# Performance work log

Measured on AMD Instinct MI355X. Metric: run time of the kernel, lower is better.

The kernel has to match this reference:

```python
import jax, jax.numpy as jnp
import numpy as np

SEQ_LEN = 16
N_NODES = 64000
N_EDGES = 1024000
FEAT = 16
H1 = 64
H2 = 64
LSTM_DIM = 128
FC1 = 64
FC2 = 3


def setup_inputs() -> dict:
    key = jax.random.key(0)
    ks = jax.random.split(key, 16)
    def w(k, shape, fan_in):
        return (jax.random.normal(k, shape, jnp.float32) / np.float32(np.sqrt(fan_in)))
    return {
        "x": jax.random.normal(ks[0], (N_NODES, FEAT), jnp.float32),
        "edge_attr": jax.random.uniform(ks[1], (N_EDGES, 1), jnp.float32),
        "W1": w(ks[2], (FEAT, H1), FEAT),
        "b1": jnp.zeros((H1,), jnp.float32),
        "W2": w(ks[3], (H1, H2), H1),
        "b2": jnp.zeros((H2,), jnp.float32),
        "W_ih": w(ks[4], (4 * LSTM_DIM, H2), H2),
        "W_hh": w(ks[5], (4 * LSTM_DIM, LSTM_DIM), LSTM_DIM),
        "b_ih": jnp.zeros((4 * LSTM_DIM,), jnp.float32),
        "b_hh": jnp.zeros((4 * LSTM_DIM,), jnp.float32),
        "fw1": w(ks[6], (LSTM_DIM, FC1), LSTM_DIM),
        "fb1": jnp.zeros((FC1,), jnp.float32),
        "fw2": w(ks[7], (FC1, FC2), FC1),
        "fb2": jnp.zeros((FC2,), jnp.float32),
        "edge_index": jax.random.randint(ks[8], (2, N_EDGES), 0, N_NODES, dtype=jnp.int64),
        "batch_size": 8,
    }


def gcn_conv(x, edge_index, ew, W, b):
    # PyG GCNConv with edge_weight: add self-loops (weight 1), symmetric norm.
    n = x.shape[0]
    row, col = edge_index[0], edge_index[1]
    lin = x @ W                                        # [N, H]
    deg = jax.ops.segment_sum(ew, col, num_segments=n) + 1.0  # self-loop weight 1
    dinv = jax.lax.rsqrt(deg)
    norm = dinv[row] * ew * dinv[col]                  # [E]
    agg = jax.ops.segment_sum(norm[:, None] * lin[row], col, num_segments=n)
    agg = agg + lin * (dinv * dinv)[:, None]           # self-loop term: 1/deg
    return agg + b


def lstm_last(x, W_ih, W_hh, b_ih, b_hh):
    # x: [B, T, D]; torch LSTM gate order i, f, g, o. Returns last hidden [B, H].
    B = x.shape[0]
    H = W_hh.shape[1]
    xg = jnp.einsum('btd,gd->btg', x, W_ih) + (b_ih + b_hh)  # [B, T, 4H]
    def step(carry, g_t):
        h, c = carry
        g = g_t + h @ W_hh.T
        i, f, gg, o = jnp.split(g, 4, axis=-1)
        c = jax.nn.sigmoid(f) * c + jax.nn.sigmoid(i) * jnp.tanh(gg)
        h = jax.nn.sigmoid(o) * jnp.tanh(c)
        return (h, c), None
    h0 = jnp.zeros((B, H), x.dtype)
    (h, _), _ = jax.lax.scan(step, (h0, h0), xg.transpose(1, 0, 2))
    return h


def reference(x, edge_attr, W1, b1, W2, b2, W_ih, W_hh, b_ih, b_hh,
              fw1, fb1, fw2, fb2, edge_index, batch_size):
    ew = edge_attr[:, 0]
    out = gcn_conv(x, edge_index, ew, W1, b1)
    out = jax.nn.relu(out)                 # dropout: identity in eval
    out = gcn_conv(out, edge_index, ew, W2, b2)
    out = jax.nn.relu(out)
    out = out.reshape(-1, SEQ_LEN, out.shape[-1])      # [B*S, T, H2]
    h = lstm_last(out, W_ih, W_hh, b_ih, b_hh)          # [B*S, LSTM]
    h = h.reshape(batch_size, -1, LSTM_DIM)             # [B, S, LSTM]
    h = jax.nn.relu(h @ fw1 + fb1)
    logits = h @ fw2 + fb2
    return jax.nn.softmax(logits, axis=2)
```

## Files before the change

kernel.cpp:

```cpp
#include <hip/hip_runtime.h>
#include <hip/hip_bf16.h>
#include <hip/hip_fp16.h>
#include <math.h>

#define NN 64000
#define NE 1024000
#define NB 4000
#define NT 16
#define LROWS 16
#define NBKT 250

typedef __attribute__((ext_vector_type(8))) short short8;
typedef __attribute__((ext_vector_type(4))) float f32x4;

__device__ __forceinline__ float fsigm(float x) {
    return __builtin_amdgcn_rcpf(1.0f + __expf(-x));
}
__device__ __forceinline__ float ftanh(float x) {
    return 1.0f - 2.0f * __builtin_amdgcn_rcpf(1.0f + __expf(2.0f * x));
}
__device__ __forceinline__ unsigned short hbits(float v) {
    __half h = __float2half(v);
    return reinterpret_cast<unsigned short&>(h);
}
__device__ __forceinline__ float hval(unsigned short b) {
    __half h;
    reinterpret_cast<unsigned short&>(h) = b;
    return __half2float(h);
}

__global__ __launch_bounds__(256) void k_zero256(int* __restrict__ p) {
    p[threadIdx.x] = 0;
}

__global__ __launch_bounds__(256) void k_bhist(const int* __restrict__ ei,
                                               int* __restrict__ bcnt) {
    __shared__ int h[256];
    int tid = threadIdx.x;
    h[tid] = 0;
    __syncthreads();
    int base = blockIdx.x * 4096;
    #pragma unroll
    for (int j = 0; j < 16; ++j) {
        int c = ei[NE + base + j * 256 + tid];
        atomicAdd(&h[c >> 8], 1);
    }
    __syncthreads();
    if (tid < NBKT && h[tid]) atomicAdd(&bcnt[tid], h[tid]);
}

__global__ __launch_bounds__(256) void k_bscan(const int* __restrict__ bcnt,
                                               int* __restrict__ bbase,
                                               int* __restrict__ bcur) {
    __shared__ int sm[256];
    int tid = threadIdx.x;
    int v = (tid < NBKT) ? bcnt[tid] : 0;
    sm[tid] = v;
    __syncthreads();
    #pragma unroll
    for (int d = 1; d < 256; d <<= 1) {
        int t = (tid >= d) ? sm[tid - d] : 0;
        __syncthreads();
        sm[tid] += t;
        __syncthreads();
    }
    if (tid < NBKT) { int ex = sm[tid] - v; bbase[tid] = ex; bcur[tid] = ex; }
    if (tid == 255) bbase[NBKT] = sm[255];
}

__global__ __launch_bounds__(256) void k_bin(const int* __restrict__ ei,
                                             const float* __restrict__ ew,
                                             int* __restrict__ bcur,
                                             uint2* __restrict__ binned) {
    __shared__ uint2 stage[4096];
    __shared__ int sm[256];
    __shared__ int lofs[256], lcur[256], ladj[256];
    int tid = threadIdx.x;
    sm[tid] = 0;
    __syncthreads();
    int base = blockIdx.x * 4096;
    int cs[16];
    #pragma unroll
    for (int j = 0; j < 16; ++j) {
        cs[j] = ei[NE + base + j * 256 + tid];
        atomicAdd(&sm[cs[j] >> 8], 1);
    }
    __syncthreads();
    int v = sm[tid];
    #pragma unroll
    for (int d = 1; d < 256; d <<= 1) {
        int t = (tid >= d) ? sm[tid - d] : 0;
        __syncthreads();
        sm[tid] += t;
        __syncthreads();
    }
    int ex = sm[tid] - v;
    lofs[tid] = ex;
    lcur[tid] = ex;
    if (tid < NBKT) ladj[tid] = atomicAdd(&bcur[tid], v) - ex;
    __syncthreads();
    #pragma unroll
    for (int j = 0; j < 16; ++j) {
        int e = base + j * 256 + tid;
        int c = cs[j];
        int b = c >> 8;
        unsigned r = (unsigned)ei[e];
        float wv = ew[e];
        int slot = atomicAdd(&lcur[b], 1);
        stage[slot] = make_uint2(r | ((unsigned)(c & 255) << 16) | ((unsigned)b << 24),
                                 __float_as_uint(wv));
    }
    __syncthreads();
    #pragma unroll
    for (int j = 0; j < 16; ++j) {
        int i = j * 256 + tid;
        uint2 rec = stage[i];
        int b = rec.x >> 24;
        binned[ladj[b] + i] = rec;
    }
}

__global__ __launch_bounds__(256) void k_csr(const uint2* __restrict__ binned,
                                             const int* __restrict__ bbase,
                                             unsigned* __restrict__ edata,
                                             int* __restrict__ off,
                                             float* __restrict__ dinv) {
    __shared__ int cnt[256];
    __shared__ float sumw[256];
    __shared__ int lcur[256];
    __shared__ int sm[256];
    int tid = threadIdx.x;
    int b = blockIdx.x;
    int s = bbase[b], e1 = bbase[b + 1];
    cnt[tid] = 0;
    sumw[tid] = 0.0f;
    __syncthreads();
    for (int i = s + tid; i < e1; i += 256) {
        uint2 rec = binned[i];
        int nl = (rec.x >> 16) & 255;
        atomicAdd(&cnt[nl], 1);
        atomicAdd(&sumw[nl], __uint_as_float(rec.y));
    }
    __syncthreads();
    int v = cnt[tid];
    sm[tid] = v;
    __syncthreads();
    #pragma unroll
    for (int d = 1; d < 256; d <<= 1) {
        int t = (tid >= d) ? sm[tid - d] : 0;
        __syncthreads();
        sm[tid] += t;
        __syncthreads();
    }
    int ex = sm[tid] - v;
    off[b * 256 + tid] = s + ex;
    dinv[b * 256 + tid] = rsqrtf(1.0f + sumw[tid]);
    lcur[tid] = ex;
    if (b == 0 && tid == 0) off[NN] = NE;
    __syncthreads();
    for (int i = s + tid; i < e1; i += 256) {
        uint2 rec = binned[i];
        int nl = (rec.x >> 16) & 255;
        int p = atomicAdd(&lcur[nl], 1);
        edata[s + p] = (rec.x & 0xFFFFu) |
                       ((unsigned)hbits(__uint_as_float(rec.y)) << 16);
    }
}

__global__ __launch_bounds__(256) void k_xh(const float* __restrict__ x,
                                            const float* __restrict__ dinv,
                                            __half* __restrict__ xh) {
    int i = blockIdx.x * 256 + threadIdx.x;
    int n = i >> 4;
    xh[i] = __float2half(x[i] * dinv[n]);
}

__global__ __launch_bounds__(256) void k_gather16(const __half* __restrict__ xh,
                                                  const unsigned* __restrict__ edata,
                                                  const int* __restrict__ off,
                                                  const float* __restrict__ dinv,
                                                  __half* __restrict__ aggx) {
    int tid = threadIdx.x;
    int lane = tid & 63;
    int wv = tid >> 6;
    int n = blockIdx.x * 4 + wv;
    int g = lane >> 3;
    int fl = lane & 7;
    const __half2* xh2 = (const __half2*)xh;
    float2 acc = make_float2(0.0f, 0.0f);
    if (g == 0) acc = __half22float2(xh2[((size_t)n << 3) + fl]);
    int s = off[n], e1 = off[n + 1];
    int e = s + g;
    for (; e + 8 < e1; e += 16) {
        unsigned d0 = edata[e];
        unsigned d1 = edata[e + 8];
        float2 l0 = __half22float2(xh2[((size_t)(d0 & 0xFFFFu) << 3) + fl]);
        float2 l1 = __half22float2(xh2[((size_t)(d1 & 0xFFFFu) << 3) + fl]);
        float w0 = hval((unsigned short)(d0 >> 16));
        float w1 = hval((unsigned short)(d1 >> 16));
        acc.x = fmaf(w0, l0.x, acc.x); acc.y = fmaf(w0, l0.y, acc.y);
        acc.x = fmaf(w1, l1.x, acc.x); acc.y = fmaf(w1, l1.y, acc.y);
    }
    if (e < e1) {
        unsigned d0 = edata[e];
        float2 l0 = __half22float2(xh2[((size_t)(d0 & 0xFFFFu) << 3) + fl]);
        float w0 = hval((unsigned short)(d0 >> 16));
        acc.x = fmaf(w0, l0.x, acc.x);
        acc.y = fmaf(w0, l0.y, acc.y);
    }
    acc.x += __shfl_xor(acc.x, 8, 64);
    acc.y += __shfl_xor(acc.y, 8, 64);
    acc.x += __shfl_xor(acc.x, 16, 64);
    acc.y += __shfl_xor(acc.y, 16, 64);
    acc.x += __shfl_xor(acc.x, 32, 64);
    acc.y += __shfl_xor(acc.y, 32, 64);
    if (g == 0) {
        float dn = dinv[n];
        ((__half2*)aggx)[((size_t)n << 3) + fl] = __floats2half2_rn(dn * acc.x, dn * acc.y);
    }
}

__global__ __launch_bounds__(256) void k_wgcn(const float* __restrict__ W1,
                                              const float* __restrict__ W2,
                                              unsigned short* __restrict__ W1f,
                                              unsigned short* __restrict__ W2f) {
    int i = blockIdx.x * 256 + threadIdx.x;
    if (i < 2048) {
        int j = i & 7, l = (i >> 3) & 63, nt = i >> 9;
        int n = nt * 16 + (l & 15);
        int k = ((l >> 4) << 3) + j;
        W1f[i] = (k < 16) ? hbits(W1[k * 64 + n]) : (unsigned short)0;
    } else if (i < 6144) {
        int i2 = i - 2048;
        int j = i2 & 7, l = (i2 >> 3) & 63, ci = i2 >> 9;
        int nt = ci & 3, ks = ci >> 2;
        int n = nt * 16 + (l & 15);
        int k = ks * 32 + ((l >> 4) << 3) + j;
        W2f[i2] = hbits(W2[k * 64 + n]);
    }
}

__global__ __launch_bounds__(256) void k_lin2f(const __half* __restrict__ aggx,
                                               const unsigned short* __restrict__ W1f,
                                               const float* __restrict__ b1,
                                               const unsigned short* __restrict__ W2f,
                                               const float* __restrict__ dinv,
                                               __half* __restrict__ linp2) {
    __shared__ unsigned short Ax[4][512];
    __shared__ unsigned short Hd[4][2][512];
    __shared__ unsigned short Ot[64 * 64];
    int tid = threadIdx.x;
    int lane = tid & 63;
    int w = tid >> 6;
    int n0 = blockIdx.x * 64;

    short8 B1[4], B2[8];
    #pragma unroll
    for (int nt = 0; nt < 4; ++nt) B1[nt] = *(const short8*)&W1f[nt * 512 + lane * 8];
    #pragma unroll
    for (int ci = 0; ci < 8; ++ci) B2[ci] = *(const short8*)&W2f[ci * 512 + lane * 8];

    {
        int idx = tid;
        ((unsigned int*)Ax)[(idx >> 7) * 256 + 128 + (idx & 127)] = 0;
        idx += 256;
        ((unsigned int*)Ax)[(idx >> 7) * 256 + 128 + (idx & 127)] = 0;
    }
    {
        int row = tid >> 2, k0 = (tid & 3) * 4;
        uint2 bits = *(const uint2*)(aggx + (size_t)(n0 + row) * 16 + k0);
        unsigned short hv[4] = {(unsigned short)(bits.x & 0xFFFF), (unsigned short)(bits.x >> 16),
                                (unsigned short)(bits.y & 0xFFFF), (unsigned short)(bits.y >> 16)};
        int wq = row >> 4, m = row & 15;
        #pragma unroll
        for (int d = 0; d < 4; ++d) {
            int k = k0 + d;
            Ax[wq][(((k >> 3) << 4) + m) * 8 + (k & 7)] = hv[d];
        }
    }
    __syncthreads();

    short8 a = *(const short8*)&Ax[w][lane * 8];
    f32x4 acc[4];
    #pragma unroll
    for (int nt = 0; nt < 4; ++nt) acc[nt] = (f32x4){0.f, 0.f, 0.f, 0.f};
    #pragma unroll
    for (int nt = 0; nt < 4; ++nt)
        acc[nt] = __builtin_amdgcn_mfma_f32_16x16x32_f16(a, B1[nt], acc[nt], 0, 0, 0);

    int rb = (lane >> 4) * 4;
    #pragma unroll
    for (int nt = 0; nt < 4; ++nt) {
        int col = nt * 16 + (lane & 15);
        float bc = b1[col];
        #pragma unroll
        for (int q = 0; q < 4; ++q) {
            float hv = fmaxf(acc[nt][q] + bc, 0.0f);
            int row = rb + q;
            Hd[w][col >> 5][((((col & 31) >> 3) << 4) + row) * 8 + (col & 7)] = hbits(hv);
        }
    }
    short8 a0 = *(const short8*)&Hd[w][0][lane * 8];
    short8 a1 = *(const short8*)&Hd[w][1][lane * 8];
    f32x4 c2[4];
    #pragma unroll
    for (int nt = 0; nt < 4; ++nt) c2[nt] = (f32x4){0.f, 0.f, 0.f, 0.f};
    #pragma unroll
    for (int nt = 0; nt < 4; ++nt)
        c2[nt] = __builtin_amdgcn_mfma_f32_16x16x32_f16(a0, B2[nt], c2[nt], 0, 0, 0);
    #pragma unroll
    for (int nt = 0; nt < 4; ++nt)
        c2[nt] = __builtin_amdgcn_mfma_f32_16x16x32_f16(a1, B2[4 + nt], c2[nt], 0, 0, 0);

    float dv[4];
    #pragma unroll
    for (int q = 0; q < 4; ++q) dv[q] = dinv[n0 + w * 16 + rb + q];
    #pragma unroll
    for (int nt = 0; nt < 4; ++nt) {
        int col = nt * 16 + (lane & 15);
        #pragma unroll
        for (int q = 0; q < 4; ++q) {
            Ot[(w * 16 + rb + q) * 64 + col] = hbits(c2[nt][q] * dv[q]);
        }
    }
    __syncthreads();
    {
        int row = tid >> 2, c0 = (tid & 3) * 16;
        short8 v0 = *(const short8*)&Ot[row * 64 + c0];
        short8 v1 = *(const short8*)&Ot[row * 64 + c0 + 8];
        *(short8*)&linp2[(size_t)(n0 + row) * 64 + c0] = v0;
        *(short8*)&linp2[(size_t)(n0 + row) * 64 + c0 + 8] = v1;
    }
}

__global__ __launch_bounds__(256) void k_gather(const __half* __restrict__ linp,
                                                const unsigned* __restrict__ edata,
                                                const int* __restrict__ off,
                                                const float* __restrict__ dinv,
                                                const float* __restrict__ bvec,
                                                __half* __restrict__ agg) {
    int tid = threadIdx.x;
    int lane = tid & 63;
    int wv = tid >> 6;
    int n = blockIdx.x * 4 + wv;
    int hf = lane >> 5;
    int fl = lane & 31;
    const __half2* lp2 = (const __half2*)linp;
    float2 acc = make_float2(0.0f, 0.0f);
    if (hf == 0) {
        acc = __half22float2(lp2[((size_t)n << 5) + fl]);
    }
    int s = off[n], e1 = off[n + 1];
    int e = s + hf;
    for (; e + 6 < e1; e += 8) {
        unsigned d0 = edata[e];
        unsigned d1 = edata[e + 2];
        unsigned d2 = edata[e + 4];
        unsigned d3 = edata[e + 6];
        float2 l0 = __half22float2(lp2[((size_t)(d0 & 0xFFFFu) << 5) + fl]);
        float2 l1 = __half22float2(lp2[((size_t)(d1 & 0xFFFFu) << 5) + fl]);
        float2 l2 = __half22float2(lp2[((size_t)(d2 & 0xFFFFu) << 5) + fl]);
        float2 l3 = __half22float2(lp2[((size_t)(d3 & 0xFFFFu) << 5) + fl]);
        float w0 = hval((unsigned short)(d0 >> 16));
        float w1 = hval((unsigned short)(d1 >> 16));
        float w2 = hval((unsigned short)(d2 >> 16));
        float w3 = hval((unsigned short)(d3 >> 16));
        acc.x = fmaf(w0, l0.x, acc.x); acc.y = fmaf(w0, l0.y, acc.y);
        acc.x = fmaf(w1, l1.x, acc.x); acc.y = fmaf(w1, l1.y, acc.y);
        acc.x = fmaf(w2, l2.x, acc.x); acc.y = fmaf(w2, l2.y, acc.y);
        acc.x = fmaf(w3, l3.x, acc.x); acc.y = fmaf(w3, l3.y, acc.y);
    }
    for (; e < e1; e += 2) {
        unsigned d0 = edata[e];
        float2 l0 = __half22float2(lp2[((size_t)(d0 & 0xFFFFu) << 5) + fl]);
        float w0 = hval((unsigned short)(d0 >> 16));
        acc.x = fmaf(w0, l0.x, acc.x);
        acc.y = fmaf(w0, l0.y, acc.y);
    }
    acc.x += __shfl_xor(acc.x, 32, 64);
    acc.y += __shfl_xor(acc.y, 32, 64);
    if (hf == 0) {
        float dn = dinv[n];
        float ox = fmaxf(fmaf(dn, acc.x, bvec[fl * 2]), 0.0f);
        float oy = fmaxf(fmaf(dn, acc.y, bvec[fl * 2 + 1]), 0.0f);
        ((__half2*)agg)[((size_t)n << 5) + fl] = __floats2half2_rn(ox, oy);
    }
}

__global__ __launch_bounds__(256) void k_wfrag(const float* __restrict__ W_ih,
                                               const float* __restrict__ W_hh,
                                               const float* __restrict__ b_ih,
                                               const float* __restrict__ b_hh,
                                               unsigned short* __restrict__ Bus,
                                               float* __restrict__ biasb) {
    int i = blockIdx.x * 256 + threadIdx.x;
    if (i < 192 * 512) {
        int j = i & 7;
        int l = (i >> 3) & 63;
        int ci = i >> 9;
        int ntg = ci & 31;
        int ks = ci >> 5;
        int col = ntg * 16 + (l & 15);
        int k = ks * 32 + ((l >> 4) << 3) + j;
        float w = (k < 64) ? W_ih[col * 64 + k] : W_hh[col * 128 + (k - 64)];
        Bus[i] = hbits(w);
    }
    if (i < 512) biasb[i] = b_ih[i] + b_hh[i];
}

__global__ __launch_bounds__(512, 2) void k_lstm(const unsigned short* __restrict__ seq,
                                                 const unsigned short* __restrict__ Bus,
                                                 const float* __restrict__ biasb,
                                                 float* __restrict__ hout) {
    __shared__ unsigned short Aus[6 * 512];
    int tid = threadIdx.x;
    int lane = tid & 63;
    int w = tid >> 6;
    int b0 = blockIdx.x * LROWS;

    int u = w * 16 + (lane & 15);
    int rbase = (lane >> 4) * 4;
    float bI = biasb[u], bF = biasb[128 + u], bG = biasb[256 + u], bO = biasb[384 + u];
    float cst[4] = {0.0f, 0.0f, 0.0f, 0.0f};

    short8 Bf[24];
    #pragma unroll
    for (int ks = 0; ks < 6; ++ks) {
        #pragma unroll
        for (int g = 0; g < 4; ++g) {
            int ci = ks * 32 + 8 * g + w;
            Bf[ks * 4 + g] = *(const short8*)&Bus[(size_t)ci * 512 + lane * 8];
        }
    }

    for (int i = tid; i < 1024; i += 512) ((unsigned int*)Aus)[512 + i] = 0;
    {
        int i0 = tid * 2;
        int row = i0 >> 6, k0 = i0 & 63;
        unsigned v = *(const unsigned*)&seq[((size_t)(b0 + row) * NT + 0) * 64 + k0];
        int ks = k0 >> 5, kr = k0 & 31;
        Aus[ks * 512 + (((kr >> 3) << 4) + row) * 8 + (kr & 7)] = (unsigned short)v;
        kr = (k0 + 1) & 31; ks = (k0 + 1) >> 5;
        Aus[ks * 512 + (((kr >> 3) << 4) + row) * 8 + (kr & 7)] = (unsigned short)(v >> 16);
    }
    __syncthreads();

    for (int t = 0; t < NT; ++t) {
        f32x4 acc[4];
        #pragma unroll
        for (int g = 0; g < 4; ++g) acc[g] = (f32x4){0.f, 0.f, 0.f, 0.f};
        #pragma unroll
        for (int ks = 0; ks < 6; ++ks) {
            short8 ah = *(const short8*)&Aus[ks * 512 + lane * 8];
            #pragma unroll
            for (int g = 0; g < 4; ++g)
                acc[g] = __builtin_amdgcn_mfma_f32_16x16x32_f16(ah, Bf[ks * 4 + g], acc[g], 0, 0, 0);
        }
        __syncthreads();

        if (t == NT - 1) {
            #pragma unroll
            for (int q = 0; q < 4; ++q) {
                float nc = fsigm(acc[1][q] + bF) * cst[q]
                         + fsigm(acc[0][q] + bI) * ftanh(acc[2][q] + bG);
                cst[q] = nc;
                float hv = fsigm(acc[3][q] + bO) * ftanh(nc);
                hout[(size_t)(b0 + rbase + q) * 128 + u] = hv;
            }
        } else {
            int kh = 64 + u;
            int ksh = kh >> 5, krh = kh & 31;
            int hbase = ksh * 512 + ((krh >> 3) << 4) * 8 + (krh & 7);
            #pragma unroll
            for (int q = 0; q < 4; ++q) {
                float nc = fsigm(acc[1][q] + bF) * cst[q]
                         + fsigm(acc[0][q] + bI) * ftanh(acc[2][q] + bG);
                cst[q] = nc;
                float hv = fsigm(acc[3][q] + bO) * ftanh(nc);
                Aus[hbase + (rbase + q) * 8] = hbits(hv);
            }
            {
                int i0 = tid * 2;
                int row = i0 >> 6, k0 = i0 & 63;
                unsigned v = *(const unsigned*)&seq[((size_t)(b0 + row) * NT + (t + 1)) * 64 + k0];
                int ks = k0 >> 5, kr = k0 & 31;
                Aus[ks * 512 + (((kr >> 3) << 4) + row) * 8 + (kr & 7)] = (unsigned short)v;
                kr = (k0 + 1) & 31; ks = (k0 + 1) >> 5;
                Aus[ks * 512 + (((kr >> 3) << 4) + row) * 8 + (kr & 7)] = (unsigned short)(v >> 16);
            }
            __syncthreads();
        }
    }
}

__global__ __launch_bounds__(256) void k_fc(const float* __restrict__ h,
                                            const float* __restrict__ fw1,
                                            const float* __restrict__ fb1,
                                            const float* __restrict__ fw2,
                                            const float* __restrict__ fb2,
                                            float* __restrict__ out) {
    __shared__ float hid[4][64];
    int tid = threadIdx.x;
    int lane = tid & 63;
    int w = tid >> 6;
    int b = blockIdx.x * 4 + w;
    const float* hr = h + b * 128;
    float acc = fb1[lane];
    #pragma unroll 4
    for (int k = 0; k < 128; ++k) acc = fmaf(hr[k], fw1[k * 64 + lane], acc);
    hid[w][lane] = fmaxf(acc, 0.0f);
    __syncthreads();
    if (lane == 0) {
        float lg[3];
        #pragma unroll
        for (int l = 0; l < 3; ++l) {
            float a = fb2[l];
            for (int j = 0; j < 64; ++j) a = fmaf(hid[w][j], fw2[j * 3 + l], a);
            lg[l] = a;
        }
        float m = fmaxf(lg[0], fmaxf(lg[1], lg[2]));
        float e0 = expf(lg[0] - m), e1 = expf(lg[1] - m), e2 = expf(lg[2] - m);
        float s = 1.0f / (e0 + e1 + e2);
        out[b * 3 + 0] = e0 * s;
        out[b * 3 + 1] = e1 * s;
        out[b * 3 + 2] = e2 * s;
    }
}

extern "C" void kernel_launch(void* const* d_in, const int* in_sizes, int n_in,
                              void* d_out, int out_size, void* d_ws, size_t ws_size,
                              hipStream_t stream) {
    const float* x    = (const float*)d_in[0];
    const float* ea   = (const float*)d_in[1];
    const float* W1   = (const float*)d_in[2];
    const float* b1   = (const float*)d_in[3];
    const float* W2   = (const float*)d_in[4];
    const float* b2   = (const float*)d_in[5];
    const float* W_ih = (const float*)d_in[6];
    const float* W_hh = (const float*)d_in[7];
    const float* b_ih = (const float*)d_in[8];
    const float* b_hh = (const float*)d_in[9];
    const float* fw1  = (const float*)d_in[10];
    const float* fb1  = (const float*)d_in[11];
    const float* fw2  = (const float*)d_in[12];
    const float* fb2  = (const float*)d_in[13];
    const int*   ei   = (const int*)d_in[14];
    float* out = (float*)d_out;

    float* ws    = (float*)d_ws;
    float* dinv  = ws;
    float* bufA  = dinv + NN;
    float* bufB  = bufA + NN * 64;
    unsigned short* Bus = (unsigned short*)(bufB + NN * 64);
    float* biasb = bufB + NN * 64 + 98304 / 2;
    float* hbuf  = biasb + 512;
    int*   bcnt  = (int*)(hbuf + NB * 128);
    int*   bbase = bcnt + 256;
    int*   bcur  = bbase + 256;
    int*   off   = bcur + 256;
    unsigned* edata = (unsigned*)(off + NN + 4);
    __half* aggx = (__half*)(edata + NE);
    __half* xh   = aggx + NN * 16;
    unsigned short* W1f = (unsigned short*)(xh + NN * 16);
    unsigned short* W2f = W1f + 2048;
    uint2* binned = (uint2*)bufA;
    __half* linp  = (__half*)bufA;
    __half* aggB  = (__half*)bufB;

    k_zero256<<<1, 256, 0, stream>>>(bcnt);
    k_bhist<<<NBKT, 256, 0, stream>>>(ei, bcnt);
    k_bscan<<<1, 256, 0, stream>>>(bcnt, bbase, bcur);
    k_bin<<<NBKT, 256, 0, stream>>>(ei, ea, bcur, binned);
    k_csr<<<NBKT, 256, 0, stream>>>(binned, bbase, edata, off, dinv);

    k_wfrag<<<384, 256, 0, stream>>>(W_ih, W_hh, b_ih, b_hh, Bus, biasb);
    k_wgcn<<<24, 256, 0, stream>>>(W1, W2, W1f, W2f);

    k_xh<<<4000, 256, 0, stream>>>(x, dinv, xh);
    k_gather16<<<16000, 256, 0, stream>>>(xh, edata, off, dinv, aggx);

    k_lin2f<<<1000, 256, 0, stream>>>(aggx, W1f, b1, W2f, dinv, linp);

    k_gather<<<16000, 256, 0, stream>>>(linp, edata, off, dinv, b2, aggB);

    k_lstm<<<250, 512, 0, stream>>>((const unsigned short*)aggB, Bus, biasb, hbuf);

    k_fc<<<1000, 256, 0, stream>>>(hbuf, fw1, fb1, fw2, fb2, out);
}
```

Baseline: 154.1 us.

## Split layer-2 gather into two 32-column planes and fuse small prep kernels

Result: slower. 176.9 us (+14.8%).

```diff
diff --git a/kernel.cpp b/kernel.cpp
--- a/kernel.cpp
+++ b/kernel.cpp
@@ -122,9 +122,11 @@
 
 __global__ __launch_bounds__(256) void k_csr(const uint2* __restrict__ binned,
                                              const int* __restrict__ bbase,
+                                             const float* __restrict__ x,
                                              unsigned* __restrict__ edata,
                                              int* __restrict__ off,
-                                             float* __restrict__ dinv) {
+                                             float* __restrict__ dinv,
+                                             __half* __restrict__ xh) {
     __shared__ int cnt[256];
     __shared__ float sumw[256];
     __shared__ int lcur[256];
@@ -154,7 +156,9 @@
     }
     int ex = sm[tid] - v;
     off[b * 256 + tid] = s + ex;
-    dinv[b * 256 + tid] = rsqrtf(1.0f + sumw[tid]);
+    float dv = rsqrtf(1.0f + sumw[tid]);
+    dinv[b * 256 + tid] = dv;
+    sumw[tid] = dv;
     lcur[tid] = ex;
     if (b == 0 && tid == 0) off[NN] = NE;
     __syncthreads();
@@ -165,14 +169,10 @@
         edata[s + p] = (rec.x & 0xFFFFu) |
                        ((unsigned)hbits(__uint_as_float(rec.y)) << 16);
     }
-}
-
-__global__ __launch_bounds__(256) void k_xh(const float* __restrict__ x,
-                                            const float* __restrict__ dinv,
-                                            __half* __restrict__ xh) {
-    int i = blockIdx.x * 256 + threadIdx.x;
-    int n = i >> 4;
-    xh[i] = __float2half(x[i] * dinv[n]);
+    size_t nb = (size_t)b * 4096;
+    for (int i = tid; i < 4096; i += 256) {
+        xh[nb + i] = __float2half(x[nb + i] * sumw[i >> 4]);
+    }
 }
 
 __global__ __launch_bounds__(256) void k_gather16(const __half* __restrict__ xh,
@@ -220,23 +220,48 @@
     }
 }
 
-__global__ __launch_bounds__(256) void k_wgcn(const float* __restrict__ W1,
-                                              const float* __restrict__ W2,
-                                              unsigned short* __restrict__ W1f,
-                                              unsigned short* __restrict__ W2f) {
-    int i = blockIdx.x * 256 + threadIdx.x;
-    if (i < 2048) {
-        int j = i & 7, l = (i >> 3) & 63, nt = i >> 9;
-        int n = nt * 16 + (l & 15);
-        int k = ((l >> 4) << 3) + j;
-        W1f[i] = (k < 16) ? hbits(W1[k * 64 + n]) : (unsigned short)0;
-    } else if (i < 6144) {
-        int i2 = i - 2048;
-        int j = i2 & 7, l = (i2 >> 3) & 63, ci = i2 >> 9;
-        int nt = ci & 3, ks = ci >> 2;
-        int n = nt * 16 + (l & 15);
-        int k = ks * 32 + ((l >> 4) << 3) + j;
-        W2f[i2] = hbits(W2[k * 64 + n]);
+__global__ __launch_bounds__(256) void k_wfrag(const float* __restrict__ W_ih,
+                                               const float* __restrict__ W_hh,
+                                               const float* __restrict__ b_ih,
+                                               const float* __restrict__ b_hh,
+                                               const float* __restrict__ W1,
+                                               const float* __restrict__ W2,
+                                               unsigned short* __restrict__ Bus,
+                                               float* __restrict__ biasb,
+                                               unsigned short* __restrict__ W1f,
+                                               unsigned short* __restrict__ W2f) {
+    int tid = threadIdx.x;
+    int blk = blockIdx.x;
+    if (blk < 384) {
+        int i = blk * 256 + tid;
+        if (i < 192 * 512) {
+            int j = i & 7;
+            int l = (i >> 3) & 63;
+            int ci = i >> 9;
+            int ntg = ci & 31;
+            int ks = ci >> 5;
+            int col = ntg * 16 + (l & 15);
+            int k = ks * 32 + ((l >> 4) << 3) + j;
+            float w = (k < 64) ? W_ih[col * 64 + k] : W_hh[col * 128 + (k - 64)];
+            Bus[i] = hbits(w);
+        }
+        if (i < 512) biasb[i] = b_ih[i] + b_hh[i];
+    } else {
+        for (int i = tid; i < 6144; i += 256) {
+            if (i < 2048) {
+                int j = i & 7, l = (i >> 3) & 63, nt = i >> 9;
+                int n = nt * 16 + (l & 15);
+                int k = ((l >> 4) << 3) + j;
+                W1f[i] = (k < 16) ? hbits(W1[k * 64 + n]) : (unsigned short)0;
+            } else {
+                int i2 = i - 2048;
+                int j = i2 & 7, l = (i2 >> 3) & 63, ci = i2 >> 9;
+                int nt = ci & 3, ks = ci >> 2;
+                int n = nt * 16 + (l & 15);
+                int k = ks * 32 + ((l >> 4) << 3) + j;
+                W2f[i2] = hbits(W2[k * 64 + n]);
+            }
+        }
     }
 }
 
@@ -245,7 +270,8 @@
                                                const float* __restrict__ b1,
                                                const unsigned short* __restrict__ W2f,
                                                const float* __restrict__ dinv,
-                                               __half* __restrict__ linp2) {
+                                               __half* __restrict__ linpA,
+                                               __half* __restrict__ linpB) {
     __shared__ unsigned short Ax[4][512];
     __shared__ unsigned short Hd[4][2][512];
     __shared__ unsigned short Ot[64 * 64];
@@ -328,39 +354,42 @@
         int row = tid >> 2, c0 = (tid & 3) * 16;
         short8 v0 = *(const short8*)&Ot[row * 64 + c0];
         short8 v1 = *(const short8*)&Ot[row * 64 + c0 + 8];
-        *(short8*)&linp2[(size_t)(n0 + row) * 64 + c0] = v0;
-        *(short8*)&linp2[(size_t)(n0 + row) * 64 + c0 + 8] = v1;
-    }
-}
-
-__global__ __launch_bounds__(256) void k_gather(const __half* __restrict__ linp,
-                                                const unsigned* __restrict__ edata,
-                                                const int* __restrict__ off,
-                                                const float* __restrict__ dinv,
-                                                const float* __restrict__ bvec,
-                                                __half* __restrict__ agg) {
+        __half* dst = (c0 < 32) ? (linpA + (size_t)(n0 + row) * 32 + c0)
+                                : (linpB + (size_t)(n0 + row) * 32 + (c0 - 32));
+        *(short8*)dst = v0;
+        *(short8*)(dst + 8) = v1;
+    }
+}
+
+__global__ __launch_bounds__(256) void k_gather32(const __half* __restrict__ plane,
+                                                  const unsigned* __restrict__ edata,
+                                                  const int* __restrict__ off,
+                                                  const float* __restrict__ dinv,
+                                                  const float* __restrict__ bvec,
+                                                  __half* __restrict__ agg,
+                                                  int cb) {
     int tid = threadIdx.x;
     int lane = tid & 63;
     int wv = tid >> 6;
     int n = blockIdx.x * 4 + wv;
-    int hf = lane >> 5;
-    int fl = lane & 31;
-    const __half2* lp2 = (const __half2*)linp;
+    int g = lane >> 4;
+    int fl = lane & 15;
+    const __half2* lp2 = (const __half2*)plane;
     float2 acc = make_float2(0.0f, 0.0f);
-    if (hf == 0) {
-        acc = __half22float2(lp2[((size_t)n << 5) + fl]);
+    if (g == 0) {
+        acc = __half22float2(lp2[((size_t)n << 4) + fl]);
     }
     int s = off[n], e1 = off[n + 1];
-    int e = s + hf;
-    for (; e + 6 < e1; e += 8) {
+    int e = s + g;
+    for (; e + 12 < e1; e += 16) {
         unsigned d0 = edata[e];
-        unsigned d1 = edata[e + 2];
-        unsigned d2 = edata[e + 4];
-        unsigned d3 = edata[e + 6];
-        float2 l0 = __half22float2(lp2[((size_t)(d0 & 0xFFFFu) << 5) + fl]);
-        float2 l1 = __half22float2(lp2[((size_t)(d1 & 0xFFFFu) << 5) + fl]);
-        float2 l2 = __half22float2(lp2[((size_t)(d2 & 0xFFFFu) << 5) + fl]);
-        float2 l3 = __half22float2(lp2[((size_t)(d3 & 0xFFFFu) << 5) + fl]);
+        unsigned d1 = edata[e + 4];
+        unsigned d2 = edata[e + 8];
+        unsigned d3 = edata[e + 12];
+        float2 l0 = __half22float2(lp2[((size_t)(d0 & 0xFFFFu) << 4) + fl]);
+        float2 l1 = __half22float2(lp2[((size_t)(d1 & 0xFFFFu) << 4) + fl]);
+        float2 l2 = __half22float2(lp2[((size_t)(d2 & 0xFFFFu) << 4) + fl]);
+        float2 l3 = __half22float2(lp2[((size_t)(d3 & 0xFFFFu) << 4) + fl]);
         float w0 = hval((unsigned short)(d0 >> 16));
         float w1 = hval((unsigned short)(d1 >> 16));
         float w2 = hval((unsigned short)(d2 >> 16));
@@ -370,42 +399,23 @@
         acc.x = fmaf(w2, l2.x, acc.x); acc.y = fmaf(w2, l2.y, acc.y);
         acc.x = fmaf(w3, l3.x, acc.x); acc.y = fmaf(w3, l3.y, acc.y);
     }
-    for (; e < e1; e += 2) {
+    for (; e < e1; e += 4) {
         unsigned d0 = edata[e];
-        float2 l0 = __half22float2(lp2[((size_t)(d0 & 0xFFFFu) << 5) + fl]);
+        float2 l0 = __half22float2(lp2[((size_t)(d0 & 0xFFFFu) << 4) + fl]);
         float w0 = hval((unsigned short)(d0 >> 16));
         acc.x = fmaf(w0, l0.x, acc.x);
         acc.y = fmaf(w0, l0.y, acc.y);
     }
+    acc.x += __shfl_xor(acc.x, 16, 64);
+    acc.y += __shfl_xor(acc.y, 16, 64);
     acc.x += __shfl_xor(acc.x, 32, 64);
     acc.y += __shfl_xor(acc.y, 32, 64);
-    if (hf == 0) {
+    if (g == 0) {
         float dn = dinv[n];
         float ox = fmaxf(fmaf(dn, acc.x, bvec[fl * 2]), 0.0f);
         float oy = fmaxf(fmaf(dn, acc.y, bvec[fl * 2 + 1]), 0.0f);
-        ((__half2*)agg)[((size_t)n << 5) + fl] = __floats2half2_rn(ox, oy);
-    }
-}
-
-__global__ __launch_bounds__(256) void k_wfrag(const float* __restrict__ W_ih,
-                                               const float* __restrict__ W_hh,
-                                               const float* __restrict__ b_ih,
-                                               const float* __restrict__ b_hh,
-                                               unsigned short* __restrict__ Bus,
-                                               float* __restrict__ biasb) {
-    int i = blockIdx.x * 256 + threadIdx.x;
-    if (i < 192 * 512) {
-        int j = i & 7;
-        int l = (i >> 3) & 63;
-        int ci = i >> 9;
-        int ntg = ci & 31;
-        int ks = ci >> 5;
-        int col = ntg * 16 + (l & 15);
-        int k = ks * 32 + ((l >> 4) << 3) + j;
-        float w = (k < 64) ? W_ih[col * 64 + k] : W_hh[col * 128 + (k - 64)];
-        Bus[i] = hbits(w);
-    }
-    if (i < 512) biasb[i] = b_ih[i] + b_hh[i];
+        ((__half2*)agg)[((size_t)n << 5) + (cb >> 1) + fl] = __floats2half2_rn(ox, oy);
+    }
 }
 
 __global__ __launch_bounds__(512, 2) void k_lstm(const unsigned short* __restrict__ seq,
@@ -564,24 +574,24 @@
     unsigned short* W1f = (unsigned short*)(xh + NN * 16);
     unsigned short* W2f = W1f + 2048;
     uint2* binned = (uint2*)bufA;
-    __half* linp  = (__half*)bufA;
+    __half* linpA = (__half*)bufA;
+    __half* linpB = linpA + NN * 32;
     __half* aggB  = (__half*)bufB;
 
     k_zero256<<<1, 256, 0, stream>>>(bcnt);
     k_bhist<<<NBKT, 256, 0, stream>>>(ei, bcnt);
     k_bscan<<<1, 256, 0, stream>>>(bcnt, bbase, bcur);
     k_bin<<<NBKT, 256, 0, stream>>>(ei, ea, bcur, binned);
-    k_csr<<<NBKT, 256, 0, stream>>>(binned, bbase, edata, off, dinv);
-
-    k_wfrag<<<384, 256, 0, stream>>>(W_ih, W_hh, b_ih, b_hh, Bus, biasb);
-    k_wgcn<<<24, 256, 0, stream>>>(W1, W2, W1f, W2f);
-
-    k_xh<<<4000, 256, 0, stream>>>(x, dinv, xh);
+    k_csr<<<NBKT, 256, 0, stream>>>(binned, bbase, x, edata, off, dinv, xh);
+
+    k_wfrag<<<385, 256, 0, stream>>>(W_ih, W_hh, b_ih, b_hh, W1, W2, Bus, biasb, W1f, W2f);
+
     k_gather16<<<16000, 256, 0, stream>>>(xh, edata, off, dinv, aggx);
 
-    k_lin2f<<<1000, 256, 0, stream>>>(aggx, W1f, b1, W2f, dinv, linp);
-
-    k_gather<<<16000, 256, 0, stream>>>(linp, edata, off, dinv, b2, aggB);
+    k_lin2f<<<1000, 256, 0, stream>>>(aggx, W1f, b1, W2f, dinv, linpA, linpB);
+
+    k_gather32<<<16000, 256, 0, stream>>>(linpA, edata, off, dinv, b2, aggB, 0);
+    k_gather32<<<16000, 256, 0, stream>>>(linpB, edata, off, dinv, b2 + 32, aggB, 32);
 
     k_lstm<<<250, 512, 0, stream>>>((const unsigned short*)aggB, Bus, biasb, hbuf);
 
```
